# Kernel tuning notes

Hardware: AMD Instinct MI355X
Metric: run time of the kernel (lower is better)

Reference implementation:

```python
import jax, jax.numpy as jnp
import numpy as np

B, T, C, NH = 32, 784, 384, 6
HD = C // NH
SCALE = float(C) ** -0.5  # source uses dim_out**-0.5, not per-head
BN_EPS = 1e-5


def _dw_bn(xs, cw, g, b, m, v, h, w):
    # xs: [B, T, C] tokens -> depthwise 3x3 conv + eval-mode BN -> [B, T, C]
    Bn, Tn, Cn = xs.shape
    img = xs.transpose(0, 2, 1).reshape(Bn, Cn, h, w)  # b (h w) c -> b c h w
    y = jax.lax.conv_general_dilated(
        img, cw, window_strides=(1, 1), padding=((1, 1), (1, 1)),
        dimension_numbers=("NCHW", "OIHW", "NCHW"), feature_group_count=Cn)
    inv = g / jnp.sqrt(v + BN_EPS)
    y = y * inv[None, :, None, None] + (b - m * inv)[None, :, None, None]
    return y.reshape(Bn, Cn, h * w).transpose(0, 2, 1)  # b c h w -> b (h w) c


def setup_inputs() -> dict:
    key = jax.random.key(0)
    ks = jax.random.split(key, 9)
    d = {"x": jax.random.normal(ks[0], (B, T, C), jnp.float32), "h": 28, "w": 28}
    for i, nm in enumerate(["q", "k", "v"]):
        d[f"conv_w_{nm}"] = jax.random.normal(ks[1 + i], (C, 1, 3, 3), jnp.float32) * 0.2
        d[f"gamma_{nm}"] = jnp.ones((C,), jnp.float32)
        d[f"beta_{nm}"] = jnp.zeros((C,), jnp.float32)
        d[f"mean_{nm}"] = jnp.zeros((C,), jnp.float32)
        d[f"var_{nm}"] = jnp.ones((C,), jnp.float32)
    d["w_q"] = jax.random.normal(ks[4], (C, C), jnp.float32) * 0.02
    d["w_k"] = jax.random.normal(ks[5], (C, C), jnp.float32) * 0.02
    d["w_v"] = jax.random.normal(ks[6], (C, C), jnp.float32) * 0.02
    d["w_proj"] = jax.random.normal(ks[7], (C, C), jnp.float32) * 0.02
    d["b_proj"] = jnp.zeros((C,), jnp.float32)
    return d


def reference(x, h, w,
              conv_w_q, gamma_q, beta_q, mean_q, var_q,
              conv_w_k, gamma_k, beta_k, mean_k, var_k,
              conv_w_v, gamma_v, beta_v, mean_v, var_v,
              w_q, w_k, w_v, w_proj, b_proj):
    qt = _dw_bn(x, conv_w_q, gamma_q, beta_q, mean_q, var_q, h, w)
    kt = _dw_bn(x, conv_w_k, gamma_k, beta_k, mean_k, var_k, h, w)
    vt = _dw_bn(x, conv_w_v, gamma_v, beta_v, mean_v, var_v, h, w)
    Bn, Tn, Cn = x.shape
    # torch Linear: y = x @ W.T; split heads: b t (h d) -> b h t d
    q = (qt @ w_q.T).reshape(Bn, Tn, NH, HD).transpose(0, 2, 1, 3)
    k = (kt @ w_k.T).reshape(Bn, Tn, NH, HD).transpose(0, 2, 1, 3)
    v = (vt @ w_v.T).reshape(Bn, Tn, NH, HD).transpose(0, 2, 1, 3)
    attn = jnp.einsum("bhld,bhtd->bhlt", q, k) * SCALE
    attn = jax.nn.softmax(attn, axis=-1)
    o = jnp.einsum("bhlt,bhtd->bhld", attn, v)
    o = o.transpose(0, 2, 1, 3).reshape(Bn, Tn, Cn)  # b h t d -> b t (h d)
    return o @ w_proj.T + b_proj
```

## Files before the change

kernel.cpp:

```cpp
#include <hip/hip_runtime.h>

typedef __attribute__((ext_vector_type(8))) short bhalf8;
typedef __attribute__((ext_vector_type(4))) float floatx4;

#define MFMA16 __builtin_amdgcn_mfma_f32_16x16x32_bf16
#define SCALE_EXP2 0.07362225f

__device__ __forceinline__ unsigned short f2bf(float f) {
  union { float fl; unsigned u; } v;
  v.fl = f;
  unsigned r = v.u + 0x7fffu + ((v.u >> 16) & 1u);
  return (unsigned short)(r >> 16);
}
__device__ __forceinline__ unsigned fbits(float f) {
  union { float fl; unsigned u; } v; v.fl = f; return v.u;
}
__device__ __forceinline__ float asfloat(unsigned u) {
  union { unsigned uu; float fl; } v; v.uu = u; return v.fl;
}

typedef const __attribute__((address_space(1))) unsigned int* gas1_t;
typedef __attribute__((address_space(3))) unsigned int* las3_t;
__device__ __forceinline__ void async16(const void* g, void* l) {
  __builtin_amdgcn_global_load_lds((gas1_t)g, (las3_t)l, 16, 0, 0);
}

struct __align__(8) us4 { unsigned short x, y, z, w; };

__global__ __launch_bounds__(256) void cvtw_prep_kernel(
    const float* __restrict__ wq, const float* __restrict__ wk,
    const float* __restrict__ wv, const float* __restrict__ wp,
    unsigned short* __restrict__ o,
    const float* __restrict__ cwq, const float* __restrict__ gq,
    const float* __restrict__ bq,  const float* __restrict__ mq,
    const float* __restrict__ vq,
    const float* __restrict__ cwk, const float* __restrict__ gk,
    const float* __restrict__ bk,  const float* __restrict__ mk,
    const float* __restrict__ vk,
    const float* __restrict__ cwv, const float* __restrict__ gv,
    const float* __restrict__ bv,  const float* __restrict__ mv,
    const float* __restrict__ vv,
    float* __restrict__ fx) {
  if (blockIdx.x < 576) {
    int i = blockIdx.x * 256 + threadIdx.x;
    o[i]          = f2bf(wq[i]);
    o[147456 + i] = f2bf(wk[i]);
    o[294912 + i] = f2bf(wv[i]);
    o[442368 + i] = f2bf(wp[i]);
    return;
  }
  const float* cw[3] = {cwq, cwk, cwv};
  const float* gg[3] = {gq, gk, gv};
  const float* bb[3] = {bq, bk, bv};
  const float* mm[3] = {mq, mk, mv};
  const float* vr[3] = {vq, vk, vv};
  for (int c = threadIdx.x; c < 384; c += 256) {
#pragma unroll
    for (int cv = 0; cv < 3; ++cv) {
#pragma unroll
      for (int i = 0; i < 9; ++i) fx[cv * 3456 + i * 384 + c] = cw[cv][c * 9 + i];
      float inv = gg[cv][c] * rsqrtf(vr[cv][c] + 1e-5f);
      fx[10368 + cv * 768 + c]       = inv;
      fx[10368 + cv * 768 + 384 + c] = bb[cv][c] - mm[cv][c] * inv;
    }
  }
}

__global__ __launch_bounds__(384) void dwconv_bn_kernel(
    const float* __restrict__ x, const float* __restrict__ fx,
    unsigned short* __restrict__ qt, unsigned short* __restrict__ kt,
    unsigned short* __restrict__ vt) {
  __shared__ __align__(16) float4 Wl[3168];
  const int tid = threadIdx.x;
  for (int i = tid; i < 3168; i += 384) Wl[i] = ((const float4*)fx)[i];
  const int tok = tid / 96;
  const int g   = tid - tok * 96;
  int blk = blockIdx.x;
  int b   = blk / 98;
  int rr  = blk - b * 98;
  int yp  = rr / 7;
  int xg  = rr - yp * 7;
  int y0  = yp * 2;
  int xx  = xg * 4 + tok;
  const float4* xv = (const float4*)x;
  float4 z4 = {0.f, 0.f, 0.f, 0.f};
  float4 tap[4][3];
#pragma unroll
  for (int dy = 0; dy < 4; ++dy)
#pragma unroll
    for (int dx = 0; dx < 3; ++dx) {
      int yy = y0 - 1 + dy, xc = xx - 1 + dx;
      bool ok = ((unsigned)yy < 28u) & ((unsigned)xc < 28u);
      tap[dy][dx] = ok ? xv[((size_t)b * 784 + yy * 28 + xc) * 96 + g] : z4;
    }
  __syncthreads();
  unsigned short* outs[3] = {qt, kt, vt};
  size_t o0 = ((size_t)b * 784 + y0 * 28 + xx) * 96 + g;
#pragma unroll
  for (int cv = 0; cv < 3; ++cv) {
    float4 s0 = z4, s1 = z4;
#pragma unroll
    for (int i = 0; i < 9; ++i) {
      int dy = i / 3, dx = i - dy * 3;
      float4 w = Wl[cv * 864 + i * 96 + g];
      float4 a = tap[dy][dx];
      float4 c = tap[dy + 1][dx];
      s0.x += a.x * w.x; s0.y += a.y * w.y; s0.z += a.z * w.z; s0.w += a.w * w.w;
      s1.x += c.x * w.x; s1.y += c.y * w.y; s1.z += c.z * w.z; s1.w += c.w * w.w;
    }
    float4 inv = Wl[2592 + cv * 192 + g];
    float4 sh  = Wl[2592 + cv * 192 + 96 + g];
    us4 o;
    o.x = f2bf(s0.x * inv.x + sh.x);
    o.y = f2bf(s0.y * inv.y + sh.y);
    o.z = f2bf(s0.z * inv.z + sh.z);
    o.w = f2bf(s0.w * inv.w + sh.w);
    ((us4*)outs[cv])[o0] = o;
    o.x = f2bf(s1.x * inv.x + sh.x);
    o.y = f2bf(s1.y * inv.y + sh.y);
    o.z = f2bf(s1.z * inv.z + sh.z);
    o.w = f2bf(s1.w * inv.w + sh.w);
    ((us4*)outs[cv])[o0 + 28 * 96] = o;
  }
}

__global__ __launch_bounds__(256) void gemm128_kernel(
    const unsigned short* __restrict__ A0, const unsigned short* __restrict__ A1,
    const unsigned short* __restrict__ A2, const unsigned short* __restrict__ wbf,
    const float* __restrict__ bias,
    unsigned short* __restrict__ qh, unsigned short* __restrict__ kh,
    unsigned short* __restrict__ vht, float* __restrict__ dout, int mode) {
  __shared__ __align__(16) unsigned short SB[17408];
  unsigned short* Al = SB;
  unsigned short* Bl = SB + 8192;
  const unsigned short* A;
  const unsigned short* W;
  int epi;
  float osc = 1.f;
  unsigned short* outb = nullptr;
  if (mode == 0) {
    int z = blockIdx.z;
    A = (z == 0) ? A0 : ((z == 1) ? A1 : A2);
    W = wbf + z * 147456;
    epi = (z == 2) ? 1 : 0;
    outb = (z == 0) ? qh : ((z == 1) ? kh : vht);
    if (z == 0) osc = SCALE_EXP2;
  } else {
    A = A0; W = wbf + 442368; epi = 2;
  }
  const int nb = blockIdx.x * 128, mb = blockIdx.y * 128;
  const int tid = threadIdx.x, lane = tid & 63;
  const int wid = tid >> 6;
  const int wr = wid >> 1, wc = wid & 1;
  const int quad = lane >> 4, l15 = lane & 15;
  floatx4 zf = {0.f, 0.f, 0.f, 0.f};
  floatx4 acc[4][4] = {{zf, zf, zf, zf}, {zf, zf, zf, zf},
                       {zf, zf, zf, zf}, {zf, zf, zf, zf}};
  for (int k0 = 0; k0 < 384; k0 += 64) {
#pragma unroll
    for (int i = 0; i < 4; ++i) {
      int chunk = tid + i * 256;
      int r = chunk >> 3, c8 = chunk & 7;
      int kcol = k0 + ((c8 ^ (r & 7)) * 8);
      async16(&A[(size_t)(mb + r) * 384 + kcol], &Al[((tid & 192) + i * 256) * 8]);
      async16(&W[(size_t)(nb + r) * 384 + kcol], &Bl[((tid & 192) + i * 256) * 8]);
    }
    __syncthreads();
    bhalf8 af[4][2], bf[4][2];
#pragma unroll
    for (int mi = 0; mi < 4; ++mi)
#pragma unroll
      for (int s = 0; s < 2; ++s) {
        int row = wr * 64 + mi * 16 + l15;
        af[mi][s] = *(const bhalf8*)&Al[row * 64 + (((s * 4 + quad) ^ (row & 7)) * 8)];
        int col = wc * 64 + mi * 16 + l15;
        bf[mi][s] = *(const bhalf8*)&Bl[col * 64 + (((s * 4 + quad) ^ (col & 7)) * 8)];
      }
#pragma unroll
    for (int mi = 0; mi < 4; ++mi)
#pragma unroll
      for (int ni = 0; ni < 4; ++ni) {
        acc[mi][ni] = MFMA16(af[mi][0], bf[ni][0], acc[mi][ni], 0, 0, 0);
        acc[mi][ni] = MFMA16(af[mi][1], bf[ni][1], acc[mi][ni], 0, 0, 0);
      }
    __syncthreads();
  }
  if (epi == 2) {
#pragma unroll
    for (int mi = 0; mi < 4; ++mi)
#pragma unroll
      for (int ni = 0; ni < 4; ++ni)
#pragma unroll
        for (int r = 0; r < 4; ++r) {
          int m = mb + wr * 64 + mi * 16 + quad * 4 + r;
          int n = nb + wc * 64 + ni * 16 + l15;
          dout[(size_t)m * 384 + n] = acc[mi][ni][r] + bias[n];
        }
  } else if (epi == 0) {
#pragma unroll
    for (int mi = 0; mi < 4; ++mi)
#pragma unroll
      for (int ni = 0; ni < 4; ++ni)
#pragma unroll
        for (int r = 0; r < 4; ++r) {
          int m = mb + wr * 64 + mi * 16 + quad * 4 + r;
          int n = nb + wc * 64 + ni * 16 + l15;
          int b = m / 784, t = m - b * 784;
          outb[(((size_t)b * 6 + (n >> 6)) * 784 + t) * 64 + (n & 63)] =
              f2bf(acc[mi][ni][r] * osc);
        }
  } else {
#pragma unroll
    for (int mi = 0; mi < 4; ++mi)
#pragma unroll
      for (int ni = 0; ni < 4; ++ni) {
        int nl = wc * 64 + ni * 16 + l15;
        int ml = wr * 64 + mi * 16 + quad * 4;
        unsigned lo = ((unsigned)f2bf(acc[mi][ni][1]) << 16) | f2bf(acc[mi][ni][0]);
        unsigned hi = ((unsigned)f2bf(acc[mi][ni][3]) << 16) | f2bf(acc[mi][ni][2]);
        uint2 pk = {lo, hi};
        *(uint2*)&SB[nl * 136 + ml] = pk;
      }
    __syncthreads();
#pragma unroll
    for (int p = 0; p < 8; ++p) {
      int idx = tid + p * 256;
      int row = idx >> 4, ck = idx & 15;
      int m0 = mb + ck * 8;
      int b = m0 / 784, t0 = m0 - b * 784;
      bhalf8 vv = *(const bhalf8*)&SB[row * 136 + ck * 8];
      *(bhalf8*)&vht[(size_t)b * 301056 + (size_t)(nb + row) * 784 + t0] = vv;
    }
  }
}

__global__ __launch_bounds__(256) void attn_kernel(
    const unsigned short* __restrict__ Q, const unsigned short* __restrict__ K,
    const unsigned short* __restrict__ Vt, unsigned short* __restrict__ O) {
  __shared__ __align__(16) unsigned short Kl[2][64 * 64];
  __shared__ __align__(16) unsigned short Vl[2][64 * 64];
  __shared__ __align__(16) unsigned short Pl[128 * 64];
  const int bh = blockIdx.x, qb = blockIdx.y * 128;
  const int tid = threadIdx.x, lane = tid & 63, wid = tid >> 6;
  const int quad = lane >> 4, l15 = lane & 15;
  const size_t hb = (size_t)bh * 50176;
  const unsigned short* Qh = Q + hb;
  const unsigned short* Kh = K + hb;
  const unsigned short* Vh = Vt + hb;

  auto stage = [&](int kb2, int bufS) {
#pragma unroll
    for (int i = 0; i < 2; ++i) {
      int c = tid + i * 256;
      int tt = c >> 3, c8 = c & 7;
      int sw = (c8 ^ (tt & 7)) * 8;
      int row = kb2 + tt; if (row > 783) row = 783;
      async16(&Kh[(size_t)row * 64 + sw], &Kl[bufS][((tid & 192) + i * 256) * 8]);
      int col = kb2 + sw; if (col > 776) col = 776;
      async16(&Vh[(size_t)tt * 784 + col], &Vl[bufS][((tid & 192) + i * 256) * 8]);
    }
  };

  bhalf8 zs = {0, 0, 0, 0, 0, 0, 0, 0};
  bhalf8 aq[2][2];
#pragma unroll
  for (int nt = 0; nt < 2; ++nt) {
    int row = qb + wid * 32 + nt * 16 + l15;
#pragma unroll
    for (int d = 0; d < 2; ++d)
      aq[nt][d] = (row < 784) ? *(const bhalf8*)&Qh[(size_t)row * 64 + d * 32 + quad * 8]
                              : zs;
  }

  floatx4 zf = {0.f, 0.f, 0.f, 0.f};
  floatx4 accO[2][4] = {{zf, zf, zf, zf}, {zf, zf, zf, zf}};
  float accL[2] = {0.f, 0.f};

  stage(0, 0);
  __syncthreads();

  for (int kt = 0; kt < 13; ++kt) {
    const int buf = kt & 1;
    const int kb = kt * 64;
    if (kt < 12) stage(kb + 64, buf ^ 1);

#pragma unroll
    for (int s = 0; s < 2; ++s) {
      if (kb + s * 32 >= 784) break;
      bhalf8 kk[2][2], vvs[4];
#pragma unroll
      for (int h = 0; h < 2; ++h)
#pragma unroll
        for (int d = 0; d < 2; ++d) {
          int tr = (2 * s + h) * 16 + l15;
          kk[h][d] = *(const bhalf8*)&Kl[buf][tr * 64 + (((d * 4 + quad) ^ (tr & 7)) * 8)];
        }
#pragma unroll
      for (int dt = 0; dt < 4; ++dt) {
        int dr = dt * 16 + l15;
        vvs[dt] = *(const bhalf8*)&Vl[buf][dr * 64 + (((s * 4 + quad) ^ (dr & 7)) * 8)];
      }
#pragma unroll
      for (int h = 0; h < 2; ++h) {
        const bool tok = (kb + (2 * s + h) * 16) < 784;
#pragma unroll
        for (int nt = 0; nt < 2; ++nt) {
          uint2 pk = {0u, 0u};
          if (tok) {
            floatx4 sf = zf;
            sf = MFMA16(kk[h][0], aq[nt][0], sf, 0, 0, 0);
            sf = MFMA16(kk[h][1], aq[nt][1], sf, 0, 0, 0);
            float p0 = exp2f(sf[0]), p1 = exp2f(sf[1]);
            float p2 = exp2f(sf[2]), p3 = exp2f(sf[3]);
            pk.x = __builtin_amdgcn_perm(fbits(p1), fbits(p0), 0x07060302u);
            pk.y = __builtin_amdgcn_perm(fbits(p3), fbits(p2), 0x07060302u);
            accL[nt] += (asfloat(fbits(p0) & 0xffff0000u) + asfloat(fbits(p1) & 0xffff0000u)) +
                        (asfloat(fbits(p2) & 0xffff0000u) + asfloat(fbits(p3) & 0xffff0000u));
          }
          int row = wid * 32 + nt * 16 + l15;
          int gr = (4 * s + 2 * h + (quad >> 1)) ^ (row & 7);
          *(uint2*)&Pl[row * 64 + gr * 8 + (quad & 1) * 4] = pk;
        }
      }
#pragma unroll
      for (int nt = 0; nt < 2; ++nt) {
        int row = wid * 32 + nt * 16 + l15;
        bhalf8 ap = *(const bhalf8*)&Pl[row * 64 + (((4 * s + quad) ^ (row & 7)) * 8)];
#pragma unroll
        for (int dt = 0; dt < 4; ++dt)
          accO[nt][dt] = MFMA16(ap, vvs[dt], accO[nt][dt], 0, 0, 0);
      }
    }
    __syncthreads();
  }

  float invq[2];
#pragma unroll
  for (int nt = 0; nt < 2; ++nt) {
    float s = accL[nt];
    s += __shfl_xor(s, 16, 64);
    s += __shfl_xor(s, 32, 64);
    invq[nt] = 1.f / s;
  }
  const int b = bh / 6, h = bh - b * 6;
#pragma unroll
  for (int qt = 0; qt < 2; ++qt)
#pragma unroll
    for (int dt = 0; dt < 4; ++dt)
#pragma unroll
      for (int r = 0; r < 4; ++r) {
        int row = qb + wid * 32 + qt * 16 + quad * 4 + r;
        if (row < 784) {
          float iv = __shfl(invq[qt], quad * 4 + r, 64);
          O[((size_t)b * 784 + row) * 384 + h * 64 + dt * 16 + l15] =
              f2bf(accO[qt][dt][r] * iv);
        }
      }
}

extern "C" void kernel_launch(void* const* d_in, const int* in_sizes, int n_in,
                              void* d_out, int out_size, void* d_ws, size_t ws_size,
                              hipStream_t stream) {
  const float* x   = (const float*)d_in[0];
  const float* cwq = (const float*)d_in[3];
  const float* gq  = (const float*)d_in[4];
  const float* bq  = (const float*)d_in[5];
  const float* mq  = (const float*)d_in[6];
  const float* vq  = (const float*)d_in[7];
  const float* cwk = (const float*)d_in[8];
  const float* gk  = (const float*)d_in[9];
  const float* bk  = (const float*)d_in[10];
  const float* mk  = (const float*)d_in[11];
  const float* vk  = (const float*)d_in[12];
  const float* cwv = (const float*)d_in[13];
  const float* gv  = (const float*)d_in[14];
  const float* bv  = (const float*)d_in[15];
  const float* mv  = (const float*)d_in[16];
  const float* vv  = (const float*)d_in[17];
  const float* wq  = (const float*)d_in[18];
  const float* wk  = (const float*)d_in[19];
  const float* wv  = (const float*)d_in[20];
  const float* wp  = (const float*)d_in[21];
  const float* bp  = (const float*)d_in[22];

  unsigned short* ws = (unsigned short*)d_ws;
  const size_t SZ = (size_t)25088 * 384;
  unsigned short* qt  = ws;
  unsigned short* ktt = ws + SZ;
  unsigned short* vtt = ws + 2 * SZ;
  unsigned short* qh  = ws + 3 * SZ;
  unsigned short* kh  = ws + 4 * SZ;
  unsigned short* vht = ws + 5 * SZ;
  unsigned short* wbf = ws + 6 * SZ;
  float* fx = (float*)(ws + 5 * SZ);
  unsigned short* ob = qt;

  cvtw_prep_kernel<<<dim3(577), dim3(256), 0, stream>>>(
      wq, wk, wv, wp, wbf,
      cwq, gq, bq, mq, vq, cwk, gk, bk, mk, vk, cwv, gv, bv, mv, vv, fx);
  dwconv_bn_kernel<<<dim3(3136), dim3(384), 0, stream>>>(x, fx, qt, ktt, vtt);
  gemm128_kernel<<<dim3(3, 196, 3), dim3(256), 0, stream>>>(
      qt, ktt, vtt, wbf, bp, qh, kh, vht, (float*)d_out, 0);
  attn_kernel<<<dim3(192, 7), dim3(256), 0, stream>>>(qh, kh, vht, ob);
  gemm128_kernel<<<dim3(3, 196, 1), dim3(256), 0, stream>>>(
      ob, ktt, vtt, wbf, bp, qh, kh, vht, (float*)d_out, 1);
}
```

Baseline: 297.7 us.

## Keep attention probabilities in registers via bpermute instead of LDS round-trip

The attention kernel no longer writes the exponentiated scores to a shared-memory P tile and reads them back. The packed bf16 probabilities are redistributed across lanes with ds_bpermute, and the PV MFMA operands are transposed so the output accumulates in a query-major layout. Row sums are now computed by an extra MFMA against a ones vector instead of masked scalar adds and shuffles, and output stores become 8-byte vectors. Launch bounds request 4 blocks per CU to use the freed LDS, at the cost of added bpermute and MFMA work and register pressure.

```diff
diff --git a/kernel.cpp b/kernel.cpp
--- a/kernel.cpp
+++ b/kernel.cpp
@@ -14,9 +14,6 @@
 }
 __device__ __forceinline__ unsigned fbits(float f) {
   union { float fl; unsigned u; } v; v.fl = f; return v.u;
-}
-__device__ __forceinline__ float asfloat(unsigned u) {
-  union { unsigned uu; float fl; } v; v.uu = u; return v.fl;
 }
 
 typedef const __attribute__((address_space(1))) unsigned int* gas1_t;
@@ -234,12 +231,11 @@
   }
 }
 
-__global__ __launch_bounds__(256) void attn_kernel(
+__global__ __launch_bounds__(256, 4) void attn_kernel(
     const unsigned short* __restrict__ Q, const unsigned short* __restrict__ K,
     const unsigned short* __restrict__ Vt, unsigned short* __restrict__ O) {
   __shared__ __align__(16) unsigned short Kl[2][64 * 64];
   __shared__ __align__(16) unsigned short Vl[2][64 * 64];
-  __shared__ __align__(16) unsigned short Pl[128 * 64];
   const int bh = blockIdx.x, qb = blockIdx.y * 128;
   const int tid = threadIdx.x, lane = tid & 63, wid = tid >> 6;
   const int quad = lane >> 4, l15 = lane & 15;
@@ -272,9 +268,13 @@
                               : zs;
   }
 
+  const int addrA = (((quad & 1) * 32) + l15) * 4;
+  const int addrB = addrA + 64;
+  const bhalf8 ones = {16256, 16256, 16256, 16256, 16256, 16256, 16256, 16256};
+
   floatx4 zf = {0.f, 0.f, 0.f, 0.f};
   floatx4 accO[2][4] = {{zf, zf, zf, zf}, {zf, zf, zf, zf}};
-  float accL[2] = {0.f, 0.f};
+  floatx4 accl[2] = {zf, zf};
 
   stage(0, 0);
   __syncthreads();
@@ -287,6 +287,7 @@
 #pragma unroll
     for (int s = 0; s < 2; ++s) {
       if (kb + s * 32 >= 784) break;
+      const bool tok1 = (kb + s * 32 + 16) < 784;
       bhalf8 kk[2][2], vvs[4];
 #pragma unroll
       for (int h = 0; h < 2; ++h)
@@ -301,61 +302,69 @@
         vvs[dt] = *(const bhalf8*)&Vl[buf][dr * 64 + (((s * 4 + quad) ^ (dr & 7)) * 8)];
       }
 #pragma unroll
-      for (int h = 0; h < 2; ++h) {
-        const bool tok = (kb + (2 * s + h) * 16) < 784;
-#pragma unroll
-        for (int nt = 0; nt < 2; ++nt) {
-          uint2 pk = {0u, 0u};
-          if (tok) {
-            floatx4 sf = zf;
-            sf = MFMA16(kk[h][0], aq[nt][0], sf, 0, 0, 0);
-            sf = MFMA16(kk[h][1], aq[nt][1], sf, 0, 0, 0);
-            float p0 = exp2f(sf[0]), p1 = exp2f(sf[1]);
-            float p2 = exp2f(sf[2]), p3 = exp2f(sf[3]);
-            pk.x = __builtin_amdgcn_perm(fbits(p1), fbits(p0), 0x07060302u);
-            pk.y = __builtin_amdgcn_perm(fbits(p3), fbits(p2), 0x07060302u);
-            accL[nt] += (asfloat(fbits(p0) & 0xffff0000u) + asfloat(fbits(p1) & 0xffff0000u)) +
-                        (asfloat(fbits(p2) & 0xffff0000u) + asfloat(fbits(p3) & 0xffff0000u));
-          }
-          int row = wid * 32 + nt * 16 + l15;
-          int gr = (4 * s + 2 * h + (quad >> 1)) ^ (row & 7);
-          *(uint2*)&Pl[row * 64 + gr * 8 + (quad & 1) * 4] = pk;
-        }
-      }
-#pragma unroll
       for (int nt = 0; nt < 2; ++nt) {
-        int row = wid * 32 + nt * 16 + l15;
-        bhalf8 ap = *(const bhalf8*)&Pl[row * 64 + (((4 * s + quad) ^ (row & 7)) * 8)];
+        uint2 pk0 = {0u, 0u}, pk1 = {0u, 0u};
+        {
+          floatx4 sf = zf;
+          sf = MFMA16(kk[0][0], aq[nt][0], sf, 0, 0, 0);
+          sf = MFMA16(kk[0][1], aq[nt][1], sf, 0, 0, 0);
+          pk0.x = __builtin_amdgcn_perm(fbits(exp2f(sf[1])), fbits(exp2f(sf[0])),
+                                        0x07060302u);
+          pk0.y = __builtin_amdgcn_perm(fbits(exp2f(sf[3])), fbits(exp2f(sf[2])),
+                                        0x07060302u);
+        }
+        if (tok1) {
+          floatx4 sf = zf;
+          sf = MFMA16(kk[1][0], aq[nt][0], sf, 0, 0, 0);
+          sf = MFMA16(kk[1][1], aq[nt][1], sf, 0, 0, 0);
+          pk1.x = __builtin_amdgcn_perm(fbits(exp2f(sf[1])), fbits(exp2f(sf[0])),
+                                        0x07060302u);
+          pk1.y = __builtin_amdgcn_perm(fbits(exp2f(sf[3])), fbits(exp2f(sf[2])),
+                                        0x07060302u);
+        }
+        unsigned wa0 = __builtin_amdgcn_ds_bpermute(addrA, (int)pk0.x);
+        unsigned wa1 = __builtin_amdgcn_ds_bpermute(addrA, (int)pk0.y);
+        unsigned wa2 = __builtin_amdgcn_ds_bpermute(addrB, (int)pk0.x);
+        unsigned wa3 = __builtin_amdgcn_ds_bpermute(addrB, (int)pk0.y);
+        unsigned wb0 = 0u, wb1 = 0u, wb2 = 0u, wb3 = 0u;
+        if (tok1) {
+          wb0 = __builtin_amdgcn_ds_bpermute(addrA, (int)pk1.x);
+          wb1 = __builtin_amdgcn_ds_bpermute(addrA, (int)pk1.y);
+          wb2 = __builtin_amdgcn_ds_bpermute(addrB, (int)pk1.x);
+          wb3 = __builtin_amdgcn_ds_bpermute(addrB, (int)pk1.y);
+        }
+        const bool hi = (quad & 2);
+        union { uint4 u; bhalf8 v; } pf;
+        pf.u.x = hi ? wb0 : wa0;
+        pf.u.y = hi ? wb1 : wa1;
+        pf.u.z = hi ? wb2 : wa2;
+        pf.u.w = hi ? wb3 : wa3;
+        accl[nt] = MFMA16(ones, pf.v, accl[nt], 0, 0, 0);
 #pragma unroll
         for (int dt = 0; dt < 4; ++dt)
-          accO[nt][dt] = MFMA16(ap, vvs[dt], accO[nt][dt], 0, 0, 0);
+          accO[nt][dt] = MFMA16(vvs[dt], pf.v, accO[nt][dt], 0, 0, 0);
       }
     }
     __syncthreads();
   }
 
-  float invq[2];
+  const int b = bh / 6, h = bh - b * 6;
 #pragma unroll
   for (int nt = 0; nt < 2; ++nt) {
-    float s = accL[nt];
-    s += __shfl_xor(s, 16, 64);
-    s += __shfl_xor(s, 32, 64);
-    invq[nt] = 1.f / s;
-  }
-  const int b = bh / 6, h = bh - b * 6;
-#pragma unroll
-  for (int qt = 0; qt < 2; ++qt)
-#pragma unroll
-    for (int dt = 0; dt < 4; ++dt)
-#pragma unroll
-      for (int r = 0; r < 4; ++r) {
-        int row = qb + wid * 32 + qt * 16 + quad * 4 + r;
-        if (row < 784) {
-          float iv = __shfl(invq[qt], quad * 4 + r, 64);
-          O[((size_t)b * 784 + row) * 384 + h * 64 + dt * 16 + l15] =
-              f2bf(accO[qt][dt][r] * iv);
-        }
-      }
+    float iv = 1.f / accl[nt][0];
+    int q = qb + wid * 32 + nt * 16 + l15;
+    if (q < 784) {
+#pragma unroll
+      for (int dt = 0; dt < 4; ++dt) {
+        us4 o;
+        o.x = f2bf(accO[nt][dt][0] * iv);
+        o.y = f2bf(accO[nt][dt][1] * iv);
+        o.z = f2bf(accO[nt][dt][2] * iv);
+        o.w = f2bf(accO[nt][dt][3] * iv);
+        *(us4*)&O[((size_t)b * 784 + q) * 384 + h * 64 + dt * 16 + quad * 4] = o;
+      }
+    }
+  }
 }
 
 extern "C" void kernel_launch(void* const* d_in, const int* in_sizes, int n_in,
```

New measurement: 297.4 us. Within noise of the previous version (-0.1%).
